# Performance work log

Hardware: AMD Instinct MI355X
Metric: run time of the kernel (lower is better)

Reference implementation:

```python
import jax, jax.numpy as jnp
import numpy as np

B, S, R = 32, 1024, 1024
HID, OUT = 512, 1024

def setup_inputs() -> dict:
    key = jax.random.key(0)
    k1, k2, k3, k4, k5, k6 = jax.random.split(key, 6)
    return {
        "representation": jax.random.normal(k1, (B, 1, R), dtype=jnp.float32),
        "size_matrix": jax.random.uniform(k2, (B, S, 1), dtype=jnp.float32),
        "W1": jax.random.normal(k3, (HID, R), dtype=jnp.float32) * 0.02,
        "b1": jax.random.normal(k4, (HID,), dtype=jnp.float32) * 0.02,
        "W2": jax.random.normal(k5, (OUT, HID), dtype=jnp.float32) * 0.02,
        "b2": jax.random.normal(k6, (OUT,), dtype=jnp.float32) * 0.02,
    }

def reference(representation, size_matrix, W1, b1, W2, b2):
    # bmm(ones_like(size_matrix)[B,S,1], representation[B,1,R]) == broadcast to [B,S,R]
    ones = jnp.ones_like(size_matrix)                       # [B,S,1]
    sized = jnp.einsum('bso,bor->bsr', ones, representation)  # [B,S,R]
    # per-position 2-layer MLP, fused into two batched GEMMs over all B*S positions
    h = jax.nn.relu(jnp.einsum('bsr,hr->bsh', sized, W1) + b1)  # [B,S,HID]
    out = jnp.einsum('bsh,oh->bso', h, W2) + b2                 # [B,S,OUT]
    return out
```

## Files before the change

### kernel.cpp

```cpp
#include <hip/hip_runtime.h>
#include <hip/hip_bf16.h>

#define BB   32
#define SS   1024
#define RR   1024
#define HID  512
#define OUTD 1024

__global__ __launch_bounds__(256) void layer1_kernel(
    const float* __restrict__ rep, const float* __restrict__ W1,
    const float* __restrict__ b1, float* __restrict__ h) {
  __shared__ float s_rep[4][RR];
  const int tid  = threadIdx.x;
  const int wave = tid >> 6;
  const int lane = tid & 63;
  const int g    = lane >> 4;
  const int l16  = lane & 15;
  const int jg   = blockIdx.x >> 3;
  const int b0   = (blockIdx.x & 7) << 2;
  const int j    = (jg << 4) + (wave << 2) + g;

  {
    const float4* src = reinterpret_cast<const float4*>(rep + (size_t)b0 * RR);
    float4* dst = reinterpret_cast<float4*>(&s_rep[0][0]);
#pragma unroll
    for (int i = 0; i < 4; ++i) dst[tid + 256 * i] = src[tid + 256 * i];
  }
  __syncthreads();

  const float4* w4 = reinterpret_cast<const float4*>(W1 + (size_t)j * RR);
  float a0 = 0.f, a1 = 0.f, a2 = 0.f, a3 = 0.f;
#pragma unroll
  for (int t = 0; t < 16; ++t) {
    const int idx = l16 + 16 * t;
    const float4 w = w4[idx];
    const float4 x0 = reinterpret_cast<const float4*>(s_rep[0])[idx];
    const float4 x1 = reinterpret_cast<const float4*>(s_rep[1])[idx];
    const float4 x2 = reinterpret_cast<const float4*>(s_rep[2])[idx];
    const float4 x3 = reinterpret_cast<const float4*>(s_rep[3])[idx];
    a0 += w.x * x0.x + w.y * x0.y + w.z * x0.z + w.w * x0.w;
    a1 += w.x * x1.x + w.y * x1.y + w.z * x1.z + w.w * x1.w;
    a2 += w.x * x2.x + w.y * x2.y + w.z * x2.z + w.w * x2.w;
    a3 += w.x * x3.x + w.y * x3.y + w.z * x3.z + w.w * x3.w;
  }
#pragma unroll
  for (int m = 1; m <= 8; m <<= 1) {
    a0 += __shfl_xor(a0, m);
    a1 += __shfl_xor(a1, m);
    a2 += __shfl_xor(a2, m);
    a3 += __shfl_xor(a3, m);
  }
  if (l16 == 0) {
    const float bb = b1[j];
    h[(size_t)b0 * HID + j]       = fmaxf(a0 + bb, 0.f);
    h[(size_t)(b0 + 1) * HID + j] = fmaxf(a1 + bb, 0.f);
    h[(size_t)(b0 + 2) * HID + j] = fmaxf(a2 + bb, 0.f);
    h[(size_t)(b0 + 3) * HID + j] = fmaxf(a3 + bb, 0.f);
  }
}

__global__ __launch_bounds__(256) void l2bcast_kernel(
    const float* __restrict__ h, const float* __restrict__ W2,
    const float* __restrict__ b2, float* __restrict__ out) {
  __shared__ float s_h[HID];
  __shared__ float s_o[64];
  const int tid = threadIdx.x;
  const int b   = blockIdx.x >> 4;
  const int kc  = blockIdx.x & 15;
  const int k0  = kc << 6;

  reinterpret_cast<float2*>(s_h)[tid] =
      reinterpret_cast<const float2*>(h + (size_t)b * HID)[tid];
  __syncthreads();

  const int gg  = tid >> 4;
  const int l16 = tid & 15;
  const float4* s_h4 = reinterpret_cast<const float4*>(s_h);
#pragma unroll
  for (int i = 0; i < 4; ++i) {
    const int k = k0 + (i << 4) + gg;
    const float4* w = reinterpret_cast<const float4*>(W2 + (size_t)k * HID);
    float acc = 0.f;
#pragma unroll
    for (int t = 0; t < 8; ++t) {
      const float4 wv = w[l16 + 16 * t];
      const float4 xv = s_h4[l16 + 16 * t];
      acc += wv.x * xv.x + wv.y * xv.y + wv.z * xv.z + wv.w * xv.w;
    }
#pragma unroll
    for (int m = 1; m <= 8; m <<= 1) acc += __shfl_xor(acc, m);
    if (l16 == 0) s_o[(i << 4) + gg] = acc + b2[k];
  }
  __syncthreads();

  const float4 v = reinterpret_cast<const float4*>(s_o)[tid & 15];
  const int r0 = tid >> 4;
  float4* __restrict__ o4 =
      reinterpret_cast<float4*>(out) + (size_t)b * SS * (OUTD / 4) + (k0 >> 2);
#pragma unroll
  for (int p = 0; p < 64; ++p) {
    const int s = r0 + (p << 4);
    o4[(size_t)s * (OUTD / 4) + (tid & 15)] = v;
  }
}

extern "C" void kernel_launch(void* const* d_in, const int* in_sizes, int n_in,
                              void* d_out, int out_size, void* d_ws, size_t ws_size,
                              hipStream_t stream) {
  const float* rep = (const float*)d_in[0];
  const float* W1 = (const float*)d_in[2];
  const float* b1 = (const float*)d_in[3];
  const float* W2 = (const float*)d_in[4];
  const float* b2 = (const float*)d_in[5];
  float* out = (float*)d_out;
  float* h   = (float*)d_ws;

  layer1_kernel<<<256, 256, 0, stream>>>(rep, W1, b1, h);
  l2bcast_kernel<<<512, 256, 0, stream>>>(h, W2, b2, out);
}
```

Before: 33.34 us.

## Fuse both MLP layers into one cooperative kernel with grid sync

Merges the layer-1 GEMV and the layer-2 GEMV plus broadcast-store kernels into a single cooperative launch of 512 blocks, separated by a grid-wide barrier. Layer 1 is re-split so each block handles 2 batch rows instead of 4, so all 512 blocks take part. This is meant to remove the second kernel launch and the inter-kernel gap. In exchange it adds the cost of a grid sync and cooperative launch, and W1 is read more times. The code falls back to the two-kernel path if the cooperative launch fails.

```diff
diff --git a/kernel.cpp b/kernel.cpp
--- a/kernel.cpp
+++ b/kernel.cpp
@@ -1,11 +1,106 @@
 #include <hip/hip_runtime.h>
-#include <hip/hip_bf16.h>
+#include <hip/hip_cooperative_groups.h>
+
+namespace cg = cooperative_groups;
 
 #define BB   32
 #define SS   1024
 #define RR   1024
 #define HID  512
 #define OUTD 1024
+
+__global__ __launch_bounds__(256) void fused_kernel(
+    const float* __restrict__ rep,
+    const float* __restrict__ W1, const float* __restrict__ b1,
+    const float* __restrict__ W2, const float* __restrict__ b2,
+    float* __restrict__ out, float* __restrict__ h) {
+  cg::grid_group grid = cg::this_grid();
+  __shared__ float s_rep[2][RR];
+  __shared__ float s_h[HID];
+  __shared__ float s_o[64];
+  const int tid  = threadIdx.x;
+  const int bid  = blockIdx.x;
+  const int wave = tid >> 6;
+  const int lane = tid & 63;
+  const int g    = lane >> 4;
+  const int l16  = lane & 15;
+
+  {
+    const int jg = bid >> 4;
+    const int b0 = (bid & 15) << 1;
+    const int j  = (jg << 4) + (wave << 2) + g;
+
+    const float4* src = reinterpret_cast<const float4*>(rep + (size_t)b0 * RR);
+    float4* dst = reinterpret_cast<float4*>(&s_rep[0][0]);
+    dst[tid]       = src[tid];
+    dst[tid + 256] = src[tid + 256];
+    __syncthreads();
+
+    const float4* w4 = reinterpret_cast<const float4*>(W1 + (size_t)j * RR);
+    const float4* x40 = reinterpret_cast<const float4*>(s_rep[0]);
+    const float4* x41 = reinterpret_cast<const float4*>(s_rep[1]);
+    float a0 = 0.f, a1 = 0.f;
+#pragma unroll
+    for (int t = 0; t < 16; ++t) {
+      const int idx = l16 + 16 * t;
+      const float4 w = w4[idx];
+      const float4 x0 = x40[idx];
+      const float4 x1 = x41[idx];
+      a0 += w.x * x0.x + w.y * x0.y + w.z * x0.z + w.w * x0.w;
+      a1 += w.x * x1.x + w.y * x1.y + w.z * x1.z + w.w * x1.w;
+    }
+#pragma unroll
+    for (int m = 1; m <= 8; m <<= 1) {
+      a0 += __shfl_xor(a0, m);
+      a1 += __shfl_xor(a1, m);
+    }
+    if (l16 == 0) {
+      const float bb = b1[j];
+      h[(size_t)b0 * HID + j]       = fmaxf(a0 + bb, 0.f);
+      h[(size_t)(b0 + 1) * HID + j] = fmaxf(a1 + bb, 0.f);
+    }
+  }
+  grid.sync();
+
+  {
+    const int b  = bid >> 4;
+    const int kc = bid & 15;
+    const int k0 = kc << 6;
+
+    reinterpret_cast<float2*>(s_h)[tid] =
+        reinterpret_cast<const float2*>(h + (size_t)b * HID)[tid];
+    __syncthreads();
+
+    const int gg = tid >> 4;
+    const float4* s_h4 = reinterpret_cast<const float4*>(s_h);
+#pragma unroll
+    for (int i = 0; i < 4; ++i) {
+      const int k = k0 + (i << 4) + gg;
+      const float4* w = reinterpret_cast<const float4*>(W2 + (size_t)k * HID);
+      float acc = 0.f;
+#pragma unroll
+      for (int t = 0; t < 8; ++t) {
+        const float4 wv = w[l16 + 16 * t];
+        const float4 xv = s_h4[l16 + 16 * t];
+        acc += wv.x * xv.x + wv.y * xv.y + wv.z * xv.z + wv.w * xv.w;
+      }
+#pragma unroll
+      for (int m = 1; m <= 8; m <<= 1) acc += __shfl_xor(acc, m);
+      if (l16 == 0) s_o[(i << 4) + gg] = acc + b2[k];
+    }
+    __syncthreads();
+
+    const float4 v = reinterpret_cast<const float4*>(s_o)[tid & 15];
+    const int r0 = tid >> 4;
+    float4* __restrict__ o4 =
+        reinterpret_cast<float4*>(out) + (size_t)b * SS * (OUTD / 4) + (k0 >> 2);
+#pragma unroll
+    for (int p = 0; p < 64; ++p) {
+      const int s = r0 + (p << 4);
+      o4[(size_t)s * (OUTD / 4) + (tid & 15)] = v;
+    }
+  }
+}
 
 __global__ __launch_bounds__(256) void layer1_kernel(
     const float* __restrict__ rep, const float* __restrict__ W1,
@@ -115,6 +210,12 @@
   float* out = (float*)d_out;
   float* h   = (float*)d_ws;
 
-  layer1_kernel<<<256, 256, 0, stream>>>(rep, W1, b1, h);
-  l2bcast_kernel<<<512, 256, 0, stream>>>(h, W2, b2, out);
-}
+  void* args[] = {(void*)&rep, (void*)&W1, (void*)&b1,
+                  (void*)&W2,  (void*)&b2, (void*)&out, (void*)&h};
+  hipError_t err = hipLaunchCooperativeKernel(
+      (void*)fused_kernel, dim3(512), dim3(256), args, 0, stream);
+  if (err != hipSuccess) {
+    layer1_kernel<<<256, 256, 0, stream>>>(rep, W1, b1, h);
+    l2bcast_kernel<<<512, 256, 0, stream>>>(h, W2, b2, out);
+  }
+}
```

Measured after the change: 81.08 us. 2.43x slower.
